# Kernel optimization log

Measured on AMD Instinct MI355X. Metric: run time of the kernel, lower is better.

The kernel has to match this reference:

```python
import jax, jax.numpy as jnp
import numpy as np
import math


def setup_inputs() -> dict:
    key = jax.random.key(0)
    k1, k2, k3 = jax.random.split(key, 3)
    B, H, T, D = 4, 16, 4096, 128
    return {
        "q": jax.random.normal(k1, (B, H, T, D), dtype=jnp.float32),
        "k": jax.random.normal(k2, (B, H, T, D), dtype=jnp.float32),
        "v": jax.random.normal(k3, (B, H, T, D), dtype=jnp.float32),
        "BS": 32,
    }


def _compress(x, block_size):
    # blockwise mean-pool along T: [B,H,T,D] -> [B,H,C,D], C = ceil(T/BS)
    B, H, T, D = x.shape
    C = math.ceil(T / block_size)
    pad = C * block_size - T
    if pad:
        x = jnp.pad(x, ((0, 0), (0, 0), (0, pad), (0, 0)))
    return x.reshape(B, H, C, block_size, D).mean(axis=3)


def reference(q, k, v, BS):
    dk = k.shape[-1]
    k_cmp = _compress(k, BS)  # [B,H,C,D]
    v_cmp = _compress(v, BS)  # [B,H,C,D]
    # scaled dot-product attention over compressed KV
    score = jnp.einsum("bhtd,bhcd->bhtc", q, k_cmp) / math.sqrt(dk)
    score = jax.nn.softmax(score, axis=-1)  # [B,H,T,C]
    out = jnp.einsum("bhtc,bhcd->bhtd", score, v_cmp)  # [B,H,T,D]
    return (out, score)
```

## Files before the change

### kernel.cpp

```cpp
#include <hip/hip_runtime.h>
#include <hip/hip_bf16.h>

typedef __attribute__((ext_vector_type(8))) short short8;
typedef __attribute__((ext_vector_type(4))) float f32x4;

#define B_  4
#define H_  16
#define T_  4096
#define D_  128
#define BS_ 32
#define C_  128
#define BH_ (B_ * H_)

__device__ __forceinline__ int posperm(int x) {
  return (x & ~31) | (((x >> 2) & 3) << 3) | (((x >> 4) & 1) << 2) | (x & 3);
}

__device__ __forceinline__ unsigned short f2bf(float f) {
  __hip_bfloat16 h = __float2bfloat16(f);
  return __builtin_bit_cast(unsigned short, h);
}

__global__ __launch_bounds__(256) void compress_kernel(
    const float* __restrict__ k, const float* __restrict__ v,
    unsigned short* __restrict__ kc, unsigned short* __restrict__ vT) {
  int blk = blockIdx.x;
  int bh  = blk >> 4;
  int cg  = blk & 15;
  int cb  = cg * 8 + (threadIdx.x >> 5);
  int l   = threadIdx.x & 31;
  const float* kp = k + ((size_t)bh * T_ + (size_t)cb * BS_) * D_ + 4 * l;
  const float* vp = v + ((size_t)bh * T_ + (size_t)cb * BS_) * D_ + 4 * l;
  float4 ks = {0.f, 0.f, 0.f, 0.f}, vs = {0.f, 0.f, 0.f, 0.f};
#pragma unroll
  for (int j = 0; j < BS_; ++j) {
    float4 a = *(const float4*)(kp + (size_t)j * D_);
    float4 b = *(const float4*)(vp + (size_t)j * D_);
    ks.x += a.x; ks.y += a.y; ks.z += a.z; ks.w += a.w;
    vs.x += b.x; vs.y += b.y; vs.z += b.z; vs.w += b.w;
  }
  const float s = 1.0f / BS_;
  size_t slab = (size_t)bh * (C_ * D_);
  unsigned short kq[4] = {f2bf(ks.x * s), f2bf(ks.y * s), f2bf(ks.z * s), f2bf(ks.w * s)};
  int p0 = posperm(4 * l) ^ ((cb & 7) << 3);
  *(uint2*)&kc[slab + (size_t)cb * D_ + p0] =
      *(const uint2*)kq;
  float vv[4] = {vs.x * s, vs.y * s, vs.z * s, vs.w * s};
#pragma unroll
  for (int i = 0; i < 4; ++i) {
    int d = 4 * l + i;
    vT[slab + (size_t)d * C_ + (posperm(cb) ^ ((d & 7) << 3))] = f2bf(vv[i]);
  }
}

__global__ __launch_bounds__(256, 2) void attn_kernel(
    const float* __restrict__ q, const unsigned short* __restrict__ kc,
    const unsigned short* __restrict__ vT, float* __restrict__ out,
    float* __restrict__ score) {
  __shared__ uint4 sbuf[4096];

  int blk    = blockIdx.x;
  int bh     = blk >> 6;
  int tchunk = blk & 63;
  int tid    = threadIdx.x;
  int wave   = tid >> 6;
  int lane   = tid & 63;
  int g      = lane >> 4;
  int lr     = lane & 15;
  int rx     = lr & 7;
  int t0     = tchunk * 64 + wave * 16;

  const uint4* kg = (const uint4*)(kc + (size_t)bh * (C_ * D_));
  const uint4* vg = (const uint4*)(vT + (size_t)bh * (C_ * D_));
#pragma unroll
  for (int it = 0; it < 8; ++it) {
    sbuf[it * 256 + tid]        = kg[it * 256 + tid];
    sbuf[2048 + it * 256 + tid] = vg[it * 256 + tid];
  }

  const float scale = 0.08838834764831845f;
  short8 qf[4];
  const float* qrow = q + ((size_t)bh * T_ + t0 + lr) * D_;
#pragma unroll
  for (int ks = 0; ks < 4; ++ks) {
    int d0 = 4 * g + 32 * ks;
    float4 a = *(const float4*)(qrow + d0);
    float4 b = *(const float4*)(qrow + d0 + 16);
    short8 f;
    f[0] = (short)f2bf(a.x * scale); f[1] = (short)f2bf(a.y * scale);
    f[2] = (short)f2bf(a.z * scale); f[3] = (short)f2bf(a.w * scale);
    f[4] = (short)f2bf(b.x * scale); f[5] = (short)f2bf(b.y * scale);
    f[6] = (short)f2bf(b.z * scale); f[7] = (short)f2bf(b.w * scale);
    qf[ks] = f;
  }
  __syncthreads();

  f32x4 accS[8];
#pragma unroll
  for (int cm = 0; cm < 8; ++cm) accS[cm] = f32x4{0.f, 0.f, 0.f, 0.f};
#pragma unroll
  for (int cm = 0; cm < 8; ++cm) {
    int rbase = (lr + 16 * cm) * 16;
#pragma unroll
    for (int ks = 0; ks < 4; ++ks) {
      uint4 kf = sbuf[rbase + ((4 * ks + g) ^ rx)];
      accS[cm] = __builtin_amdgcn_mfma_f32_16x16x32_bf16(
          __builtin_bit_cast(short8, kf), qf[ks], accS[cm], 0, 0, 0);
    }
  }

  float m = -3.0e38f;
#pragma unroll
  for (int cm = 0; cm < 8; ++cm)
#pragma unroll
    for (int r = 0; r < 4; ++r) m = fmaxf(m, accS[cm][r]);
  m = fmaxf(m, __shfl_xor(m, 16));
  m = fmaxf(m, __shfl_xor(m, 32));

  float sum = 0.f;
#pragma unroll
  for (int cm = 0; cm < 8; ++cm) {
#pragma unroll
    for (int r = 0; r < 4; ++r) {
      float p = __expf(accS[cm][r] - m);
      accS[cm][r] = p;
      sum += p;
    }
  }
  sum += __shfl_xor(sum, 16);
  sum += __shfl_xor(sum, 32);
  float inv = 1.0f / sum;
#pragma unroll
  for (int cm = 0; cm < 8; ++cm)
#pragma unroll
    for (int r = 0; r < 4; ++r) accS[cm][r] *= inv;

  __syncthreads();

  float* bw = (float*)sbuf + wave * 2048;
#pragma unroll
  for (int cm = 0; cm < 8; ++cm) {
    int c4 = (g + 4 * cm) ^ rx;
    *(f32x4*)&bw[lr * 128 + c4 * 4] = accS[cm];
  }
  float* dstS = score + ((size_t)bh * T_ + t0) * C_;
#pragma unroll
  for (int j = 0; j < 8; ++j) {
    int row = 2 * j + (lane >> 5);
    int c4  = lane & 31;
    f32x4 val = *(const f32x4*)&bw[row * 128 + (c4 ^ (row & 7)) * 4];
    *(f32x4*)&dstS[(size_t)row * C_ + c4 * 4] = val;
  }

  short8 pf[4];
#pragma unroll
  for (int ks = 0; ks < 4; ++ks) {
    short8 f;
#pragma unroll
    for (int r = 0; r < 4; ++r) {
      f[r]     = (short)f2bf(accS[2 * ks][r]);
      f[4 + r] = (short)f2bf(accS[2 * ks + 1][r]);
    }
    pf[ks] = f;
  }

  const uint4* vbuf = sbuf + 2048;
#pragma unroll
  for (int nt = 0; nt < 8; ++nt) {
    f32x4 o = f32x4{0.f, 0.f, 0.f, 0.f};
    int rbase = (lr + 16 * nt) * 16;
#pragma unroll
    for (int ks = 0; ks < 4; ++ks) {
      uint4 vf = vbuf[rbase + ((4 * ks + g) ^ rx)];
      o = __builtin_amdgcn_mfma_f32_16x16x32_bf16(
          __builtin_bit_cast(short8, vf), pf[ks], o, 0, 0, 0);
    }
    int c4 = (g + 4 * nt) ^ rx;
    *(f32x4*)&bw[lr * 128 + c4 * 4] = o;
  }
  float* dstO = out + ((size_t)bh * T_ + t0) * D_;
#pragma unroll
  for (int j = 0; j < 8; ++j) {
    int row = 2 * j + (lane >> 5);
    int c4  = lane & 31;
    f32x4 val = *(const f32x4*)&bw[row * 128 + (c4 ^ (row & 7)) * 4];
    *(f32x4*)&dstO[(size_t)row * D_ + c4 * 4] = val;
  }
}

extern "C" void kernel_launch(void* const* d_in, const int* in_sizes, int n_in,
                              void* d_out, int out_size, void* d_ws, size_t ws_size,
                              hipStream_t stream) {
  const float* q = (const float*)d_in[0];
  const float* k = (const float*)d_in[1];
  const float* v = (const float*)d_in[2];
  float* out   = (float*)d_out;
  float* score = out + (size_t)BH_ * T_ * D_;

  unsigned short* kc = (unsigned short*)d_ws;
  unsigned short* vT = kc + (size_t)BH_ * C_ * D_;

  compress_kernel<<<BH_ * 16, 256, 0, stream>>>(k, v, kc, vT);
  attn_kernel<<<BH_ * 64, 256, 0, stream>>>(q, kc, vT, out, score);
}
```

Baseline: 148.0 us.

## Use 512-thread attention blocks with halved per-wave staging buffers

The attention kernel now runs 8 waves per block and covers 128 query rows per block, so each compressed K/V slab loaded into LDS is shared by twice as many rows. The per-wave LDS staging for score and output writeback is cut to half-width tiles written in two passes, which keeps the 64KB shared buffer within size with 8 waves. Launch bounds request 4 blocks per CU, which is likely not reachable given 64KB of LDS per block, and the added register pressure could spill.

```diff
diff --git a/kernel.cpp b/kernel.cpp
--- a/kernel.cpp
+++ b/kernel.cpp
@@ -43,8 +43,7 @@
   size_t slab = (size_t)bh * (C_ * D_);
   unsigned short kq[4] = {f2bf(ks.x * s), f2bf(ks.y * s), f2bf(ks.z * s), f2bf(ks.w * s)};
   int p0 = posperm(4 * l) ^ ((cb & 7) << 3);
-  *(uint2*)&kc[slab + (size_t)cb * D_ + p0] =
-      *(const uint2*)kq;
+  *(uint2*)&kc[slab + (size_t)cb * D_ + p0] = *(const uint2*)kq;
   float vv[4] = {vs.x * s, vs.y * s, vs.z * s, vs.w * s};
 #pragma unroll
   for (int i = 0; i < 4; ++i) {
@@ -53,29 +52,29 @@
   }
 }
 
-__global__ __launch_bounds__(256, 2) void attn_kernel(
+__global__ __launch_bounds__(512, 4) void attn_kernel(
     const float* __restrict__ q, const unsigned short* __restrict__ kc,
     const unsigned short* __restrict__ vT, float* __restrict__ out,
     float* __restrict__ score) {
   __shared__ uint4 sbuf[4096];
 
   int blk    = blockIdx.x;
-  int bh     = blk >> 6;
-  int tchunk = blk & 63;
+  int bh     = blk >> 5;
+  int tchunk = blk & 31;
   int tid    = threadIdx.x;
   int wave   = tid >> 6;
   int lane   = tid & 63;
   int g      = lane >> 4;
   int lr     = lane & 15;
   int rx     = lr & 7;
-  int t0     = tchunk * 64 + wave * 16;
+  int t0     = tchunk * 128 + wave * 16;
 
   const uint4* kg = (const uint4*)(kc + (size_t)bh * (C_ * D_));
   const uint4* vg = (const uint4*)(vT + (size_t)bh * (C_ * D_));
 #pragma unroll
-  for (int it = 0; it < 8; ++it) {
-    sbuf[it * 256 + tid]        = kg[it * 256 + tid];
-    sbuf[2048 + it * 256 + tid] = vg[it * 256 + tid];
+  for (int it = 0; it < 4; ++it) {
+    sbuf[it * 512 + tid]        = kg[it * 512 + tid];
+    sbuf[2048 + it * 512 + tid] = vg[it * 512 + tid];
   }
 
   const float scale = 0.08838834764831845f;
@@ -137,19 +136,22 @@
 
   __syncthreads();
 
-  float* bw = (float*)sbuf + wave * 2048;
-#pragma unroll
-  for (int cm = 0; cm < 8; ++cm) {
-    int c4 = (g + 4 * cm) ^ rx;
-    *(f32x4*)&bw[lr * 128 + c4 * 4] = accS[cm];
-  }
+  float* bw = (float*)sbuf + wave * 1024;
   float* dstS = score + ((size_t)bh * T_ + t0) * C_;
 #pragma unroll
-  for (int j = 0; j < 8; ++j) {
-    int row = 2 * j + (lane >> 5);
-    int c4  = lane & 31;
-    f32x4 val = *(const f32x4*)&bw[row * 128 + (c4 ^ (row & 7)) * 4];
-    *(f32x4*)&dstS[(size_t)row * C_ + c4 * 4] = val;
+  for (int h = 0; h < 2; ++h) {
+#pragma unroll
+    for (int cq = 0; cq < 4; ++cq) {
+      int c4 = (g + 4 * cq) ^ rx;
+      *(f32x4*)&bw[lr * 64 + c4 * 4] = accS[4 * h + cq];
+    }
+#pragma unroll
+    for (int j = 0; j < 4; ++j) {
+      int row = 4 * j + (lane >> 4);
+      int cq  = lane & 15;
+      f32x4 val = *(const f32x4*)&bw[row * 64 + (cq ^ (row & 7)) * 4];
+      *(f32x4*)&dstS[(size_t)row * C_ + 64 * h + cq * 4] = val;
+    }
   }
 
   short8 pf[4];
@@ -165,26 +167,30 @@
   }
 
   const uint4* vbuf = sbuf + 2048;
-#pragma unroll
-  for (int nt = 0; nt < 8; ++nt) {
-    f32x4 o = f32x4{0.f, 0.f, 0.f, 0.f};
-    int rbase = (lr + 16 * nt) * 16;
-#pragma unroll
-    for (int ks = 0; ks < 4; ++ks) {
-      uint4 vf = vbuf[rbase + ((4 * ks + g) ^ rx)];
-      o = __builtin_amdgcn_mfma_f32_16x16x32_bf16(
-          __builtin_bit_cast(short8, vf), pf[ks], o, 0, 0, 0);
-    }
-    int c4 = (g + 4 * nt) ^ rx;
-    *(f32x4*)&bw[lr * 128 + c4 * 4] = o;
-  }
   float* dstO = out + ((size_t)bh * T_ + t0) * D_;
 #pragma unroll
-  for (int j = 0; j < 8; ++j) {
-    int row = 2 * j + (lane >> 5);
-    int c4  = lane & 31;
-    f32x4 val = *(const f32x4*)&bw[row * 128 + (c4 ^ (row & 7)) * 4];
-    *(f32x4*)&dstO[(size_t)row * D_ + c4 * 4] = val;
+  for (int h = 0; h < 2; ++h) {
+#pragma unroll
+    for (int ntq = 0; ntq < 4; ++ntq) {
+      int nt = 4 * h + ntq;
+      f32x4 o = f32x4{0.f, 0.f, 0.f, 0.f};
+      int rbase = (lr + 16 * nt) * 16;
+#pragma unroll
+      for (int ks = 0; ks < 4; ++ks) {
+        uint4 vf = vbuf[rbase + ((4 * ks + g) ^ rx)];
+        o = __builtin_amdgcn_mfma_f32_16x16x32_bf16(
+            __builtin_bit_cast(short8, vf), pf[ks], o, 0, 0, 0);
+      }
+      int c4 = (g + 4 * ntq) ^ rx;
+      *(f32x4*)&bw[lr * 64 + c4 * 4] = o;
+    }
+#pragma unroll
+    for (int j = 0; j < 4; ++j) {
+      int row = 4 * j + (lane >> 4);
+      int cq  = lane & 15;
+      f32x4 val = *(const f32x4*)&bw[row * 64 + (cq ^ (row & 7)) * 4];
+      *(f32x4*)&dstO[(size_t)row * D_ + 64 * h + cq * 4] = val;
+    }
   }
 }
 
@@ -201,5 +207,5 @@
   unsigned short* vT = kc + (size_t)BH_ * C_ * D_;
 
   compress_kernel<<<BH_ * 16, 256, 0, stream>>>(k, v, kc, vT);
-  attn_kernel<<<BH_ * 64, 256, 0, stream>>>(q, kc, vT, out, score);
-}
+  attn_kernel<<<BH_ * 32, 512, 0, stream>>>(q, kc, vT, out, score);
+}
```

Measured after the change: 152.9 us. 3.3% more time.
